# Kernel optimization log

Hardware: AMD Instinct MI355X
Metric: run time of the kernel (lower is better)

Reference implementation:

```python
import jax, jax.numpy as jnp
import numpy as np

B, N, M, D = 64, 512, 512, 2
BLUR, SCALING, DIAMETER, P = 0.01, 0.9, 4.0, 2


def _eps_schedule():
    # geomloss epsilon_schedule: geometric decay of temperature eps = sigma^p
    # from diameter^p down to blur^p with ratio scaling^p.
    e = np.arange(P * np.log(DIAMETER), P * np.log(BLUR), P * np.log(SCALING))
    return np.concatenate([[DIAMETER ** P], np.exp(e), [BLUR ** P]]).astype(np.float32)


def setup_inputs() -> dict:
    key = jax.random.key(0)
    k1, k2, k3, k4, k5 = jax.random.split(key, 5)
    a = jax.random.uniform(k1, (B, N), dtype=jnp.float32)
    a = a / a.sum(-1, keepdims=True)  # probability weights of measure 1
    b = jax.random.uniform(k2, (B, M), dtype=jnp.float32)
    b = b / b.sum(-1, keepdims=True)  # probability weights of measure 2
    x = jax.random.normal(k3, (B, N, D), dtype=jnp.float32)
    y = jax.random.normal(k4, (B, M, D), dtype=jnp.float32)
    w = jax.random.uniform(k5, (B,), dtype=jnp.float32)  # per-sample weights
    return {"prob1": a, "coord1": x, "prob2": b, "coord2": y, "weights": w}


def _softmin(eps, C, h):
    # softmin_eps(C, h)_i = -eps * log sum_j exp(h_j - C_ij / eps)
    # C: [B,N,M], h: [B,M] -> [B,N]
    return -eps * jax.nn.logsumexp(h[:, None, :] - C / eps, axis=2)


def reference(prob1, coord1, prob2, coord2, weights):
    a, x, b, y = prob1, coord1, prob2, coord2
    # p=2 cost: C(x,y) = |x-y|^2 / 2 (geomloss convention)
    C_xy = 0.5 * jnp.sum((x[:, :, None, :] - y[:, None, :, :]) ** 2, axis=-1)  # [B,N,M]
    C_yx = jnp.swapaxes(C_xy, 1, 2)  # [B,M,N]
    a_log = jnp.log(a)
    b_log = jnp.log(b)

    eps_arr = jnp.asarray(_eps_schedule())
    eps0 = eps_arr[0]
    # initialization at the coarsest temperature
    f = _softmin(eps0, C_xy, b_log)  # [B,N] dual potential on x
    g = _softmin(eps0, C_yx, a_log)  # [B,M] dual potential on y

    def step(carry, eps):
        f, g = carry
        ft = _softmin(eps, C_xy, b_log + g / eps)
        gt = _softmin(eps, C_yx, a_log + f / eps)
        return (0.5 * (f + ft), 0.5 * (g + gt)), None

    (f, g), _ = jax.lax.scan(step, (f, g), eps_arr)

    # geomloss runs the loop without grad and does one last extrapolation step
    f = jax.lax.stop_gradient(f)
    g = jax.lax.stop_gradient(g)
    eps_last = jnp.float32(BLUR ** P)
    f_fin = _softmin(eps_last, C_xy, b_log + g / eps_last)
    g_fin = _softmin(eps_last, C_yx, a_log + f / eps_last)

    # OT_eps(a, b) = <a, f> + <b, g>  (debias=False)
    batch_loss = jnp.sum(a * f_fin, axis=-1) + jnp.sum(b * g_fin, axis=-1)  # [B]
    return jnp.sum(batch_loss * weights)
```

## Files before the change

kernel.cpp:

```cpp
#include <hip/hip_runtime.h>
#include <cmath>

#define B_ 64
#define NP 512

constexpr float L2E  = 1.4426950408889634f;
constexpr float LN2f = 0.6931471805599453f;

struct EpsList { float e[64]; };

__device__ __forceinline__ float exp2_fast(float v) {
#if __has_builtin(__builtin_amdgcn_exp2f)
    return __builtin_amdgcn_exp2f(v);
#else
    return exp2f(v);
#endif
}
__device__ __forceinline__ float log2_fast(float v) {
#if __has_builtin(__builtin_amdgcn_logf)
    return __builtin_amdgcn_logf(v);
#else
    return log2f(v);
#endif
}
__device__ __forceinline__ float max3f(float a, float b, float c) {
    return fmaxf(fmaxf(a, b), c);
}

__global__ __launch_bounds__(256, 4) void sinkhorn_pers(
    const float* __restrict__ a, const float* __restrict__ x,
    const float* __restrict__ bb, const float* __restrict__ y,
    float* __restrict__ fA, float* __restrict__ gA,
    float* __restrict__ fB, float* __restrict__ gB,
    unsigned int* __restrict__ bar, float* __restrict__ part2,
    EpsList el, int n_eps)
{
    __shared__ float4 sd[NP];
    __shared__ float s_eps[64];
    __shared__ float swred[4];

    const int bid = blockIdx.x;
    const int b   = bid & 63;
    const int q   = bid >> 6;
    const bool gside = q >= 8;
    const int rq  = q & 7;
    const int tid = threadIdx.x;
    const int sx  = tid & 7;
    const int rowbase = rq * 64 + (tid >> 3) * 2;
    unsigned int* own_ctr  = bar + b * 64 + (gside ? 32 : 0);
    unsigned int* othr_ctr = bar + b * 64 + (gside ? 0 : 32);

    if (tid < 64) s_eps[tid] = el.e[tid];

    const float2* oc2   = (const float2*)(gside ? (x + b * NP * 2) : (y + b * NP * 2));
    const float*  oprob = gside ? (a + b * NP) : (bb + b * NP);
    float ocx[2], ocy[2], on2[2], olw[2];
    #pragma unroll
    for (int u = 0; u < 2; ++u) {
        float2 c = oc2[tid + u * 256];
        ocx[u] = c.x; ocy[u] = c.y;
        on2[u] = fmaf(c.y, c.y, c.x * c.x);
        olw[u] = L2E * logf(oprob[tid + u * 256]);
    }
    const float* mcoord = gside ? (y + b * NP * 2) : (x + b * NP * 2);
    const float* mprob  = gside ? (bb + b * NP)    : (a + b * NP);
    const float4 rc01 = *(const float4*)(mcoord + rowbase * 2);
    const float x0[2] = {rc01.x, rc01.z};
    const float x1[2] = {rc01.y, rc01.w};
    float half_n2[2];
    #pragma unroll
    for (int r = 0; r < 2; ++r) half_n2[r] = 0.5f * fmaf(x1[r], x1[r], x0[r] * x0[r]);

    float pv[2];
    const int n_pass = n_eps + 2;
    __syncthreads();

    for (int p = 0; p < n_pass; ++p) {
        const float eps = (p == 0) ? s_eps[0]
                        : (p <= n_eps ? s_eps[p - 1] : s_eps[n_eps - 1]);
        const float inv_eps = 1.0f / eps;
        const float ieL2E = inv_eps * L2E;
        const float nie   = -0.5f * ieL2E;

        {
            float* opot = (gside ? ((p & 1) ? fA : fB)
                                 : ((p & 1) ? gA : gB)) + b * NP;
            #pragma unroll
            for (int u = 0; u < 2; ++u) {
                int t = tid + u * 256;
                float pot = (p != 0)
                    ? __hip_atomic_load(opot + t, __ATOMIC_RELAXED, __HIP_MEMORY_SCOPE_AGENT)
                    : 0.0f;
                float h2 = fmaf(pot, ieL2E, olw[u]);
                sd[t] = make_float4(ocx[u], ocy[u], fmaf(nie, on2[u], h2), 0.0f);
            }
        }
        __syncthreads();

        float x0p[2], x1p[2], m[2], s[2];
        #pragma unroll
        for (int r = 0; r < 2; ++r) {
            x0p[r] = x0[r] * ieL2E;
            x1p[r] = x1[r] * ieL2E;
            m[r] = -INFINITY;
            s[r] = 0.0f;
        }

        #pragma unroll 1
        for (int k = 0; k < 8; ++k) {
            float4 cj[8];
            #pragma unroll
            for (int u = 0; u < 8; ++u) cj[u] = sd[64 * k + 8 * u + sx];
            #pragma unroll
            for (int r = 0; r < 2; ++r) {
                float arg[8];
                #pragma unroll
                for (int u = 0; u < 8; ++u)
                    arg[u] = fmaf(x1p[r], cj[u].y, fmaf(x0p[r], cj[u].x, cj[u].z));
                float t0 = max3f(arg[0], arg[1], arg[2]);
                float t1 = max3f(arg[3], arg[4], arg[5]);
                float t2 = max3f(arg[6], arg[7], m[r]);
                float mn = max3f(t0, t1, t2);
                s[r] *= exp2_fast(m[r] - mn);
                #pragma unroll
                for (int u = 0; u < 8; ++u) s[r] += exp2_fast(arg[u] - mn);
                m[r] = mn;
            }
        }

        float val[2];
        #pragma unroll
        for (int r = 0; r < 2; ++r) {
            float mr = m[r];
            #pragma unroll
            for (int d = 1; d <= 4; d <<= 1) mr = fmaxf(mr, __shfl_xor(mr, d));
            float sr = s[r] * exp2_fast(m[r] - mr);
            #pragma unroll
            for (int d = 1; d <= 4; d <<= 1) sr += __shfl_xor(sr, d);
            val[r] = fmaf(-eps * LN2f, mr + log2_fast(sr), half_n2[r]);
        }

        if (p >= 1 && p <= n_eps) {
            #pragma unroll
            for (int r = 0; r < 2; ++r) val[r] = 0.5f * (pv[r] + val[r]);
        }
        #pragma unroll
        for (int r = 0; r < 2; ++r) pv[r] = val[r];

        if (p == n_pass - 1) break;

        if (sx == 0) {
            float* dst = (gside ? ((p & 1) ? gB : gA)
                                : ((p & 1) ? fB : fA)) + b * NP + rowbase;
            #pragma unroll
            for (int r = 0; r < 2; ++r)
                __hip_atomic_store(dst + r, val[r], __ATOMIC_RELAXED,
                                   __HIP_MEMORY_SCOPE_AGENT);
        }

        __syncthreads();
        if (tid == 0) {
            __hip_atomic_fetch_add(own_ctr, 1u, __ATOMIC_RELAXED,
                                   __HIP_MEMORY_SCOPE_AGENT);
            const unsigned int target = 8u * (unsigned int)(p + 1);
            unsigned int guard = 0;
            while (__hip_atomic_load(othr_ctr, __ATOMIC_RELAXED,
                                     __HIP_MEMORY_SCOPE_AGENT) < target) {
                __builtin_amdgcn_s_sleep(1);
                if (++guard > (1u << 20)) break;
            }
        }
        __syncthreads();
    }

    float local = 0.0f;
    if (sx == 0) {
        const float2 pr = *(const float2*)(mprob + rowbase);
        local = pr.x * pv[0] + pr.y * pv[1];
    }
    #pragma unroll
    for (int o = 32; o > 0; o >>= 1) local += __shfl_down(local, o);
    if ((tid & 63) == 0) swred[tid >> 6] = local;
    __syncthreads();
    if (tid == 0) part2[bid] = swred[0] + swred[1] + swred[2] + swred[3];
}

__global__ void finred_k(const float* __restrict__ part2,
                         const float* __restrict__ w, float* __restrict__ out) {
    int b = threadIdx.x;
    float s = 0.0f;
    #pragma unroll
    for (int u = 0; u < 16; ++u) s += part2[u * 64 + b];
    s *= w[b];
    #pragma unroll
    for (int o = 32; o > 0; o >>= 1) s += __shfl_down(s, o);
    if (b == 0) out[0] = s;
}

extern "C" void kernel_launch(void* const* d_in, const int* in_sizes, int n_in,
                              void* d_out, int out_size, void* d_ws, size_t ws_size,
                              hipStream_t stream) {
    const float* a  = (const float*)d_in[0];
    const float* x  = (const float*)d_in[1];
    const float* bb = (const float*)d_in[2];
    const float* y  = (const float*)d_in[3];
    const float* w  = (const float*)d_in[4];
    float* out = (float*)d_out;

    unsigned char* wsb = (unsigned char*)d_ws;
    unsigned int* bar = (unsigned int*)wsb;
    float* part2 = (float*)(wsb + 64 * 64 * 4);
    float* fA = (float*)(wsb + 64 * 64 * 4 + 1024 * 4);
    const int NB = B_ * NP;
    float* gA = fA + NB;
    float* fB = gA + NB;
    float* gB = fB + NB;

    EpsList el{};
    int n_eps = 0;
    {
        const double start = 2.0 * std::log(4.0);
        const double stop  = 2.0 * std::log(0.01);
        const double step  = 2.0 * std::log(0.9);
        el.e[n_eps++] = 16.0f;
        for (int k = 0;; ++k) {
            double v = start + (double)k * step;
            if (!(v > stop)) break;
            el.e[n_eps++] = (float)std::exp(v);
        }
        el.e[n_eps++] = (float)(0.01 * 0.01);
    }

    hipMemsetAsync(bar, 0, 64 * 64 * 4, stream);

    sinkhorn_pers<<<dim3(B_ * 16), dim3(256), 0, stream>>>(
        a, x, bb, y, fA, gA, fB, gB, bar, part2, el, n_eps);

    finred_k<<<1, 64, 0, stream>>>(part2, w, out);
}
```

Baseline: 445.7 us.

## Sort points by x-coordinate and skip negligible column chunks in softmin

A new bitonic-sort kernel orders each batch's points by their first coordinate. The persistent Sinkhorn kernel then reads coordinates, weights and potentials in that sorted order, so each 64-column chunk is spatially coherent. Inside the log-sum-exp loop, a chunk is skipped when, for every lane in the wavefront, its maximum exponent lies more than 40 (log2 units) below the running maximum. Such chunks contribute below fp32 resolution, so the exp2 work can be avoided, especially at small epsilon. This costs an extra kernel launch, gathered loads, and a wave-wide vote per chunk.

```diff
diff --git a/kernel.cpp b/kernel.cpp
--- a/kernel.cpp
+++ b/kernel.cpp
@@ -6,6 +6,7 @@
 
 constexpr float L2E  = 1.4426950408889634f;
 constexpr float LN2f = 0.6931471805599453f;
+constexpr float SKIP_T = 40.0f;
 
 struct EpsList { float e[64]; };
 
@@ -27,11 +28,56 @@
     return fmaxf(fmaxf(a, b), c);
 }
 
+__global__ __launch_bounds__(256) void sort_k(
+    const float* __restrict__ x, const float* __restrict__ y,
+    unsigned short* __restrict__ permx, unsigned short* __restrict__ permy)
+{
+    __shared__ float key[NP];
+    __shared__ int   val[NP];
+    const int tid = threadIdx.x;
+    const int b   = blockIdx.x & 63;
+    const bool yside = blockIdx.x >= 64;
+    const float* c = (yside ? y : x) + b * NP * 2;
+    #pragma unroll
+    for (int u = 0; u < 2; ++u) {
+        int t = tid + u * 256;
+        key[t] = c[2 * t];
+        val[t] = t;
+    }
+    for (int k = 2; k <= NP; k <<= 1) {
+        for (int j = k >> 1; j > 0; j >>= 1) {
+            __syncthreads();
+            #pragma unroll
+            for (int u = 0; u < 2; ++u) {
+                int i = tid + u * 256;
+                int ixj = i ^ j;
+                if (ixj > i) {
+                    bool up = ((i & k) == 0);
+                    float ki = key[i], kj = key[ixj];
+                    if ((ki > kj) == up) {
+                        key[i] = kj; key[ixj] = ki;
+                        int vi = val[i]; val[i] = val[ixj]; val[ixj] = vi;
+                    }
+                }
+            }
+        }
+    }
+    __syncthreads();
+    unsigned short* perm = (yside ? permy : permx) + b * NP;
+    #pragma unroll
+    for (int u = 0; u < 2; ++u) {
+        int t = tid + u * 256;
+        perm[t] = (unsigned short)val[t];
+    }
+}
+
 __global__ __launch_bounds__(256, 4) void sinkhorn_pers(
     const float* __restrict__ a, const float* __restrict__ x,
     const float* __restrict__ bb, const float* __restrict__ y,
     float* __restrict__ fA, float* __restrict__ gA,
     float* __restrict__ fB, float* __restrict__ gB,
+    const unsigned short* __restrict__ permx,
+    const unsigned short* __restrict__ permy,
     unsigned int* __restrict__ bar, float* __restrict__ part2,
     EpsList el, int n_eps)
 {
@@ -52,21 +98,27 @@
 
     if (tid < 64) s_eps[tid] = el.e[tid];
 
+    const unsigned short* osort = (gside ? permx : permy) + b * NP;
+    const unsigned short* msort = (gside ? permy : permx) + b * NP;
+
     const float2* oc2   = (const float2*)(gside ? (x + b * NP * 2) : (y + b * NP * 2));
     const float*  oprob = gside ? (a + b * NP) : (bb + b * NP);
     float ocx[2], ocy[2], on2[2], olw[2];
     #pragma unroll
     for (int u = 0; u < 2; ++u) {
-        float2 c = oc2[tid + u * 256];
+        int jo = osort[tid + u * 256];
+        float2 c = oc2[jo];
         ocx[u] = c.x; ocy[u] = c.y;
         on2[u] = fmaf(c.y, c.y, c.x * c.x);
-        olw[u] = L2E * logf(oprob[tid + u * 256]);
-    }
-    const float* mcoord = gside ? (y + b * NP * 2) : (x + b * NP * 2);
-    const float* mprob  = gside ? (bb + b * NP)    : (a + b * NP);
-    const float4 rc01 = *(const float4*)(mcoord + rowbase * 2);
-    const float x0[2] = {rc01.x, rc01.z};
-    const float x1[2] = {rc01.y, rc01.w};
+        olw[u] = L2E * logf(oprob[jo]);
+    }
+    const float2* mc2  = (const float2*)(gside ? (y + b * NP * 2) : (x + b * NP * 2));
+    const float* mprob = gside ? (bb + b * NP)    : (a + b * NP);
+    const int r0 = msort[rowbase], r1 = msort[rowbase + 1];
+    const float2 c0 = mc2[r0];
+    const float2 c1 = mc2[r1];
+    const float x0[2] = {c0.x, c1.x};
+    const float x1[2] = {c0.y, c1.y};
     float half_n2[2];
     #pragma unroll
     for (int r = 0; r < 2; ++r) half_n2[r] = 0.5f * fmaf(x1[r], x1[r], x0[r] * x0[r]);
@@ -119,8 +171,10 @@
                     arg[u] = fmaf(x1p[r], cj[u].y, fmaf(x0p[r], cj[u].x, cj[u].z));
                 float t0 = max3f(arg[0], arg[1], arg[2]);
                 float t1 = max3f(arg[3], arg[4], arg[5]);
-                float t2 = max3f(arg[6], arg[7], m[r]);
-                float mn = max3f(t0, t1, t2);
+                float t2 = fmaxf(arg[6], arg[7]);
+                float cmax = max3f(t0, t1, t2);
+                if (__all(cmax <= m[r] - SKIP_T)) continue;
+                float mn = fmaxf(m[r], cmax);
                 s[r] *= exp2_fast(m[r] - mn);
                 #pragma unroll
                 for (int u = 0; u < 8; ++u) s[r] += exp2_fast(arg[u] - mn);
@@ -175,8 +229,7 @@
 
     float local = 0.0f;
     if (sx == 0) {
-        const float2 pr = *(const float2*)(mprob + rowbase);
-        local = pr.x * pv[0] + pr.y * pv[1];
+        local = mprob[r0] * pv[0] + mprob[r1] * pv[1];
     }
     #pragma unroll
     for (int o = 32; o > 0; o >>= 1) local += __shfl_down(local, o);
@@ -215,6 +268,8 @@
     float* gA = fA + NB;
     float* fB = gA + NB;
     float* gB = fB + NB;
+    unsigned short* permx = (unsigned short*)(gB + NB);
+    unsigned short* permy = permx + NB;
 
     EpsList el{};
     int n_eps = 0;
@@ -233,8 +288,10 @@
 
     hipMemsetAsync(bar, 0, 64 * 64 * 4, stream);
 
+    sort_k<<<dim3(128), dim3(256), 0, stream>>>(x, y, permx, permy);
+
     sinkhorn_pers<<<dim3(B_ * 16), dim3(256), 0, stream>>>(
-        a, x, bb, y, fA, gA, fB, gB, bar, part2, el, n_eps);
+        a, x, bb, y, fA, gA, fB, gB, permx, permy, bar, part2, el, n_eps);
 
     finred_k<<<1, 64, 0, stream>>>(part2, w, out);
 }
```

Result: slower. 490.2 us (+10.0%).
